# Performance work log

Hardware: AMD Instinct MI355X
Metric: run time of the kernel (lower is better)

The kernel has to match this reference:

```python
import jax, jax.numpy as jnp
import numpy as np

B, T, D, H, L = 2, 2048, 2048, 16, 64
HD = D // H  # 128
EPS = 1e-5


def setup_inputs() -> dict:
    key = jax.random.key(0)
    ks = jax.random.split(key, 16)
    s = 0.02
    inp = {
        'x': jax.random.normal(ks[0], (B, T, D), jnp.float32),
        'mask': jnp.tril(jnp.ones((T, T), dtype=bool)),
        'ln_w': jnp.ones((D,), jnp.float32),
        'ln_b': jnp.zeros((D,), jnp.float32),
        'wq': jax.random.normal(ks[1], (D, D), jnp.float32) * s,
        'bq': jnp.zeros((D,), jnp.float32),
        'wk': jax.random.normal(ks[2], (D, D), jnp.float32) * s,
        'bk': jnp.zeros((D,), jnp.float32),
        'wv': jax.random.normal(ks[3], (D, D), jnp.float32) * s,
        'bv': jnp.zeros((D,), jnp.float32),
        'wo': jax.random.normal(ks[4], (D, D), jnp.float32) * s,
        'bo': jnp.zeros((D,), jnp.float32),
        'wcq': jax.random.normal(ks[5], (HD, L), jnp.float32) * s,
        'bcq': jnp.zeros((L,), jnp.float32),
        'wck': jax.random.normal(ks[6], (HD, L), jnp.float32) * s,
        'bck': jnp.zeros((L,), jnp.float32),
        'wcv': jax.random.normal(ks[7], (HD, L), jnp.float32) * s,
        'bcv': jnp.zeros((L,), jnp.float32),
        'wd': jax.random.normal(ks[8], (L, HD), jnp.float32) * s,
        'bd': jnp.zeros((HD,), jnp.float32),
    }
    # standard RoPE frequency table: theta_i = 10000^{-2i/HD}
    inv_freq = 1.0 / (10000.0 ** (jnp.arange(0, HD, 2, dtype=jnp.float32) / HD))
    ang = jnp.arange(T, dtype=jnp.float32)[:, None] * inv_freq[None, :]  # [T, HD/2]
    inp['freqs_cos'] = jnp.cos(ang)
    inp['freqs_sin'] = jnp.sin(ang)
    return inp


def _rope(x, cos, sin):
    # x: [B,T,H,HD]; cos/sin: [T, HD/2]; interleaved (even=real, odd=imag)
    xr, xi = x[..., 0::2], x[..., 1::2]
    c = cos[None, :, None, :]
    sn = sin[None, :, None, :]
    out_r = xr * c - xi * sn
    out_i = xr * sn + xi * c
    return jnp.stack([out_r, out_i], axis=-1).reshape(x.shape)


def reference(x, mask, freqs_cos, freqs_sin, ln_w, ln_b, wq, bq, wk, bk, wv, bv,
              wo, bo, wcq, bcq, wck, bck, wcv, bcv, wd, bd):
    # LayerNorm
    mu = jnp.mean(x, axis=-1, keepdims=True)
    var = jnp.mean(jnp.square(x - mu), axis=-1, keepdims=True)
    xn = (x - mu) / jnp.sqrt(var + EPS) * ln_w + ln_b

    q = (xn @ wq + bq).reshape(B, T, H, HD)
    k = (xn @ wk + bk).reshape(B, T, H, HD)
    v = (xn @ wv + bv).reshape(B, T, H, HD)

    q, k = _rope(q, freqs_cos, freqs_sin), _rope(k, freqs_cos, freqs_sin)

    # compress each head to the latent dim
    q_lat = q @ wcq + bcq  # [B,T,H,L]
    k_lat = k @ wck + bck
    v_lat = v @ wcv + bcv

    scale = 1.0 / np.sqrt(L).astype(np.float32)
    scores = jnp.einsum('bqhl,bkhl->bhqk', q_lat, k_lat) * scale  # [B,H,T,T]
    additive = jnp.where(mask, 0.0, -1e9).astype(scores.dtype)  # bool mask -> additive
    scores = scores + additive[None, None, :, :]
    attn = jax.nn.softmax(scores, axis=-1)

    out = jnp.einsum('bhqk,bkhl->bqhl', attn, v_lat)  # [B,T,H,L]
    out = (out @ wd + bd).reshape(B, T, D)  # decompress to head_dim, merge heads
    return out @ wo + bo
```

## Files before the change

kernel.cpp:

```cpp
#include <hip/hip_runtime.h>
#include <hip/hip_bf16.h>
#include <stdint.h>

#define BB 2
#define TB 2048
#define DB 2048
#define HB 16
#define HDB 128
#define LB 64
#define MB 4096

typedef __hip_bfloat16 bf16;
typedef __attribute__((ext_vector_type(8))) short bf16x8;
typedef __attribute__((ext_vector_type(4))) float f32x4;

#define MFMA_16x16x32 __builtin_amdgcn_mfma_f32_16x16x32_bf16

typedef __attribute__((address_space(3))) void lds_t;
typedef const __attribute__((address_space(1))) void gvm_t;

static __device__ __forceinline__ float bf2f(bf16 h) { return __bfloat162float(h); }
static __device__ __forceinline__ bf16 f2bf(float f) { return __float2bfloat16(f); }
union BV8 { bf16x8 v; bf16 e[8]; };
static __device__ __forceinline__ float bfel(bf16x8 v, int e) { BV8 u; u.v = v; return bf2f(u.e[e]); }

#define SWZC(r) (((r) ^ ((r) >> 3)) & 7)

__global__ __launch_bounds__(256) void ln_kernel(const float* __restrict__ x,
                                                 const float* __restrict__ g,
                                                 const float* __restrict__ be,
                                                 bf16* __restrict__ xn) {
  int row = blockIdx.x, tid = threadIdx.x;
  const float4* xr = (const float4*)(x + (size_t)row * DB);
  float4 a = xr[2 * tid], b = xr[2 * tid + 1];
  float s = a.x + a.y + a.z + a.w + b.x + b.y + b.z + b.w;
  float s2 = a.x * a.x + a.y * a.y + a.z * a.z + a.w * a.w +
             b.x * b.x + b.y * b.y + b.z * b.z + b.w * b.w;
  for (int off = 32; off > 0; off >>= 1) {
    s += __shfl_down(s, off);
    s2 += __shfl_down(s2, off);
  }
  __shared__ float red[8];
  int w = tid >> 6, lane = tid & 63;
  if (lane == 0) { red[w] = s; red[4 + w] = s2; }
  __syncthreads();
  s = red[0] + red[1] + red[2] + red[3];
  s2 = red[4] + red[5] + red[6] + red[7];
  float mu = s * (1.f / DB);
  float var = s2 * (1.f / DB) - mu * mu;
  float rstd = rsqrtf(var + 1e-5f);
  const float4* gw = (const float4*)g;
  const float4* bb = (const float4*)be;
  float4 g0 = gw[2 * tid], g1 = gw[2 * tid + 1];
  float4 b0 = bb[2 * tid], b1 = bb[2 * tid + 1];
  BV8 u;
  u.e[0] = f2bf((a.x - mu) * rstd * g0.x + b0.x);
  u.e[1] = f2bf((a.y - mu) * rstd * g0.y + b0.y);
  u.e[2] = f2bf((a.z - mu) * rstd * g0.z + b0.z);
  u.e[3] = f2bf((a.w - mu) * rstd * g0.w + b0.w);
  u.e[4] = f2bf((b.x - mu) * rstd * g1.x + b1.x);
  u.e[5] = f2bf((b.y - mu) * rstd * g1.y + b1.y);
  u.e[6] = f2bf((b.z - mu) * rstd * g1.z + b1.z);
  u.e[7] = f2bf((b.w - mu) * rstd * g1.w + b1.w);
  *(bf16x8*)(xn + (size_t)row * DB + tid * 8) = u.v;
}

__global__ __launch_bounds__(256) void wconv_kernel(const float* __restrict__ W,
                                                    bf16* __restrict__ Wt) {
  __shared__ float t[32][33];
  int c0 = blockIdx.x * 32, r0 = blockIdx.y * 32;
  int tx = threadIdx.x & 31, ty = threadIdx.x >> 5;
  for (int p = 0; p < 4; ++p)
    t[ty + 8 * p][tx] = W[(size_t)(r0 + ty + 8 * p) * DB + c0 + tx];
  __syncthreads();
  for (int p = 0; p < 4; ++p)
    Wt[(size_t)(c0 + ty + 8 * p) * DB + r0 + tx] = f2bf(t[tx][ty + 8 * p]);
}

__global__ __launch_bounds__(256) void fold_v_kernel(const float* __restrict__ wv,
                                                     const float* __restrict__ wcv,
                                                     bf16* __restrict__ BtV) {
  __shared__ float wvs[128][36];
  int tid = threadIdx.x;
  int k0 = blockIdx.x * 128, h = blockIdx.y;
  int l = tid & 63, ks = tid >> 6;
  float acc[32];
#pragma unroll
  for (int i = 0; i < 32; ++i) acc[i] = 0.f;
  for (int dc = 0; dc < 128; dc += 32) {
    __syncthreads();
    for (int i = tid; i < 128 * 32; i += 256) {
      int kk = i >> 5, dd = i & 31;
      wvs[kk][dd] = wv[(size_t)(k0 + kk) * DB + h * 128 + dc + dd];
    }
    __syncthreads();
    float wr[32];
#pragma unroll
    for (int dd = 0; dd < 32; ++dd) wr[dd] = wcv[(dc + dd) * 64 + l];
#pragma unroll
    for (int i = 0; i < 32; ++i) {
      const float4* row = (const float4*)&wvs[ks * 32 + i][0];
#pragma unroll
      for (int d4 = 0; d4 < 8; ++d4) {
        float4 w4 = row[d4];
        acc[i] += w4.x * wr[d4 * 4] + w4.y * wr[d4 * 4 + 1] +
                  w4.z * wr[d4 * 4 + 2] + w4.w * wr[d4 * 4 + 3];
      }
    }
  }
  bf16* dst = BtV + (size_t)(h * 64 + l) * DB + k0 + ks * 32;
#pragma unroll
  for (int i8 = 0; i8 < 4; ++i8) {
    BV8 u;
#pragma unroll
    for (int j = 0; j < 8; ++j) u.e[j] = f2bf(acc[i8 * 8 + j]);
    *(bf16x8*)(dst + i8 * 8) = u.v;
  }
}

__global__ __launch_bounds__(256) void fold_o_kernel(const float* __restrict__ wo,
                                                     const float* __restrict__ wd,
                                                     bf16* __restrict__ BtO) {
  __shared__ float wos[32][132];
  int tid = threadIdx.x;
  int n0 = blockIdx.x * 128, h = blockIdx.y;
  int l = tid & 63, ns = tid >> 6;
  float acc[32];
#pragma unroll
  for (int i = 0; i < 32; ++i) acc[i] = 0.f;
  for (int dc = 0; dc < 128; dc += 32) {
    __syncthreads();
    for (int i = tid; i < 32 * 128; i += 256) {
      int dd = i >> 7, nn = i & 127;
      wos[dd][nn] = wo[(size_t)(h * 128 + dc + dd) * DB + n0 + nn];
    }
    __syncthreads();
    float wr[32];
#pragma unroll
    for (int d4 = 0; d4 < 8; ++d4) {
      float4 w4 = *(const float4*)&wd[l * 128 + dc + d4 * 4];
      wr[d4 * 4] = w4.x; wr[d4 * 4 + 1] = w4.y;
      wr[d4 * 4 + 2] = w4.z; wr[d4 * 4 + 3] = w4.w;
    }
#pragma unroll
    for (int dd = 0; dd < 32; ++dd) {
      float w = wr[dd];
      const float4* row = (const float4*)&wos[dd][ns * 32];
#pragma unroll
      for (int i4 = 0; i4 < 8; ++i4) {
        float4 a4 = row[i4];
        acc[i4 * 4 + 0] += a4.x * w; acc[i4 * 4 + 1] += a4.y * w;
        acc[i4 * 4 + 2] += a4.z * w; acc[i4 * 4 + 3] += a4.w * w;
      }
    }
  }
#pragma unroll
  for (int i = 0; i < 32; ++i)
    BtO[(size_t)(n0 + ns * 32 + i) * 1024 + h * 64 + l] = f2bf(acc[i]);
}

__global__ __launch_bounds__(256) void biasv_kernel(const float* __restrict__ bv,
                                                    const float* __restrict__ wcv,
                                                    const float* __restrict__ bcv,
                                                    float* __restrict__ bvlat) {
  int j = blockIdx.x * 256 + threadIdx.x;
  int h = j >> 6, l = j & 63;
  float s = bcv[l];
  for (int d = 0; d < 128; ++d) s += bv[h * 128 + d] * wcv[d * 64 + l];
  bvlat[j] = s;
}

__global__ __launch_bounds__(256) void biaso_kernel(const float* __restrict__ bd,
                                                    const float* __restrict__ wo,
                                                    const float* __restrict__ bo,
                                                    float* __restrict__ bo2) {
  __shared__ float red[4][64];
  int t = threadIdx.x;
  int nl = t & 63, ks = t >> 6;
  int n = blockIdx.x * 64 + nl;
  float s = 0.f;
  for (int k = ks * 512; k < ks * 512 + 512; ++k)
    s += bd[k & 127] * wo[(size_t)k * DB + n];
  red[ks][nl] = s;
  __syncthreads();
  if (ks == 0) bo2[n] = bo[n] + red[0][nl] + red[1][nl] + red[2][nl] + red[3][nl];
}

__global__ __launch_bounds__(256) void gemm_qkv_kernel(
    const bf16* __restrict__ A, const bf16* __restrict__ wqkT,
    const bf16* __restrict__ BtV,
    const float* __restrict__ bq, const float* __restrict__ bk,
    const float* __restrict__ bvl,
    const float* __restrict__ wcq, const float* __restrict__ wck,
    const float* __restrict__ bcq, const float* __restrict__ bck,
    bf16* __restrict__ qlat, bf16* __restrict__ klat, bf16* __restrict__ vlatT,
    const float* __restrict__ fcos, const float* __restrict__ fsin) {
  constexpr int K = DB;
  __shared__ __align__(16) char smem[49152];
  bf16* As = (bf16*)smem;
  bf16* Bs = (bf16*)(smem + 8192);
  bf16* Qt = (bf16*)smem;
  bf16* Wt = (bf16*)(smem + 32768);
  int tid = threadIdx.x;
  int m0 = blockIdx.y * 128, n0 = blockIdx.x * 128;
  int w = tid >> 6, l = tid & 63;
  int wr = w >> 1, wc = w & 1;
  int lrow = l & 15, lk = (l >> 4) * 8, ck = l >> 4;
  const bf16* Bsrc = (n0 < 4096) ? (wqkT + (size_t)n0 * K)
                                 : (BtV + (size_t)(n0 - 4096) * K);
  int sel = n0 >> 11;

  if (sel < 2) {
    const float* wcp = sel == 0 ? wcq : wck;
    for (int i = tid; i < 8192; i += 256) {
      int d = i >> 6, j = i & 63;
      Wt[j * 128 + (((d >> 3) ^ (j & 7)) * 8) + (d & 7)] = f2bf(wcp[d * 64 + j]);
    }
  }

  f32x4 zero4 = {0.f, 0.f, 0.f, 0.f};
  f32x4 acc[4][4];
  for (int m = 0; m < 4; ++m)
    for (int n = 0; n < 4; ++n) acc[m][n] = zero4;

  for (int kk = 0; kk < K / 32; ++kk) {
    int k0 = kk * 32;
    __syncthreads();
#pragma unroll
    for (int i = 0; i < 2; ++i) {
      int c = i * 256 + tid;
      int r = c >> 2, cc = c & 3;
      int cb = i * 256 + (tid & ~63);
      __builtin_amdgcn_global_load_lds(
          (gvm_t*)&A[(size_t)(m0 + r) * K + k0 + cc * 8], (lds_t*)&As[cb * 8], 16, 0, 0);
      __builtin_amdgcn_global_load_lds(
          (gvm_t*)&Bsrc[(size_t)r * K + k0 + cc * 8], (lds_t*)&Bs[cb * 8], 16, 0, 0);
    }
    __syncthreads();
    bf16x8 af[4], bfr[4];
    for (int m = 0; m < 4; ++m)
      af[m] = *(bf16x8*)&As[(wr * 64 + m * 16 + lrow) * 32 + lk];
    for (int n = 0; n < 4; ++n)
      bfr[n] = *(bf16x8*)&Bs[(wc * 64 + n * 16 + lrow) * 32 + lk];
    for (int m = 0; m < 4; ++m)
      for (int n = 0; n < 4; ++n)
        acc[m][n] = MFMA_16x16x32(af[m], bfr[n], acc[m][n], 0, 0, 0);
  }

  int rg = 4 * (l >> 4), cl = l & 15;
  if (sel == 2) {
    for (int mf = 0; mf < 4; ++mf) {
      int rowb = m0 + wr * 64 + mf * 16 + rg;
      for (int nf = 0; nf < 4; ++nf) {
        int col = n0 + wc * 64 + nf * 16 + cl;
        int colV = col - 4096;
        float bv_ = bvl[colV];
        size_t vbase = ((size_t)((rowb >> 11) * HB + (colV >> 6)) * 64 + (colV & 63)) * TB
                       + (rowb & (TB - 1));
        for (int r = 0; r < 4; ++r)
          vlatT[vbase + r] = f2bf(acc[mf][nf][r] + bv_);
      }
    }
    return;
  }

  const float* bias = sel == 0 ? bq : bk;
  __syncthreads();
  for (int mf = 0; mf < 4; ++mf) {
    int rowb = m0 + wr * 64 + mf * 16 + rg;
    int rl0 = wr * 64 + mf * 16 + rg;
    for (int nf = 0; nf < 4; ++nf) {
      int col = n0 + wc * 64 + nf * 16 + cl;
      int colL = col & 2047;
      int cloc = wc * 64 + nf * 16 + cl;
      float bv_ = bias[colL];
      for (int r = 0; r < 4; ++r) {
        int rr = rowb + r;
        float v = acc[mf][nf][r] + bv_;
        float pv = __shfl_xor(v, 1);
        int t = rr & (TB - 1);
        int pi = (col & 127) >> 1;
        float c = fcos[t * 64 + pi], sn = fsin[t * 64 + pi];
        v = (col & 1) ? (pv * sn + v * c) : (v * c - pv * sn);
        int rl = rl0 + r;
        Qt[rl * 128 + ((((cloc >> 3) ^ (rl & 7)) * 8) + (cloc & 7))] = f2bf(v);
      }
    }
  }
  __syncthreads();
  f32x4 pacc[2][4];
#pragma unroll
  for (int mi = 0; mi < 2; ++mi)
#pragma unroll
    for (int nf = 0; nf < 4; ++nf) pacc[mi][nf] = zero4;
#pragma unroll
  for (int kc = 0; kc < 4; ++kc) {
    bf16x8 aq[2], bw[4];
#pragma unroll
    for (int mi = 0; mi < 2; ++mi) {
      int row = w * 32 + mi * 16 + lrow;
      aq[mi] = *(bf16x8*)&Qt[row * 128 + (((kc * 4 + ck) ^ (row & 7)) * 8)];
    }
#pragma unroll
    for (int nf = 0; nf < 4; ++nf) {
      int jrow = nf * 16 + lrow;
      bw[nf] = *(bf16x8*)&Wt[jrow * 128 + (((kc * 4 + ck) ^ (jrow & 7)) * 8)];
    }
#pragma unroll
    for (int mi = 0; mi < 2; ++mi)
#pragma unroll
      for (int nf = 0; nf < 4; ++nf)
        pacc[mi][nf] = MFMA_16x16x32(aq[mi], bw[nf], pacc[mi][nf], 0, 0, 0);
  }
  int head = (n0 & 2047) >> 7;
  const float* bias2 = sel == 0 ? bcq : bck;
  bf16* outp = sel == 0 ? qlat : klat;
#pragma unroll
  for (int mi = 0; mi < 2; ++mi)
#pragma unroll
    for (int nf = 0; nf < 4; ++nf) {
      int colj = nf * 16 + cl;
      float b2 = bias2[colj];
#pragma unroll
      for (int r = 0; r < 4; ++r) {
        int roG = m0 + w * 32 + mi * 16 + rg + r;
        outp[((size_t)roG * HB + head) * 64 + colj] = f2bf(pacc[mi][nf][r] + b2);
      }
    }
}

__global__ __launch_bounds__(256) void gemm_out_kernel(
    const bf16* __restrict__ A, const bf16* __restrict__ Bt,
    const float* __restrict__ bias, float* __restrict__ Cout) {
  constexpr int K = 1024, N = DB;
  __shared__ __align__(16) bf16 As[128 * 32];
  __shared__ __align__(16) bf16 Bs[128 * 32];
  int tid = threadIdx.x;
  int m0 = blockIdx.y * 128, n0 = blockIdx.x * 128;
  int w = tid >> 6, l = tid & 63;
  int wr = w >> 1, wc = w & 1;
  int lrow = l & 15, lk = (l >> 4) * 8;

  f32x4 zero4 = {0.f, 0.f, 0.f, 0.f};
  f32x4 acc[4][4];
  for (int m = 0; m < 4; ++m)
    for (int n = 0; n < 4; ++n) acc[m][n] = zero4;

  for (int kk = 0; kk < K / 32; ++kk) {
    int k0 = kk * 32;
    __syncthreads();
#pragma unroll
    for (int i = 0; i < 2; ++i) {
      int c = i * 256 + tid;
      int r = c >> 2, cc = c & 3;
      int cb = i * 256 + (tid & ~63);
      __builtin_amdgcn_global_load_lds(
          (gvm_t*)&A[(size_t)(m0 + r) * K + k0 + cc * 8], (lds_t*)&As[cb * 8], 16, 0, 0);
      __builtin_amdgcn_global_load_lds(
          (gvm_t*)&Bt[(size_t)(n0 + r) * K + k0 + cc * 8], (lds_t*)&Bs[cb * 8], 16, 0, 0);
    }
    __syncthreads();
    bf16x8 af[4], bfr[4];
    for (int m = 0; m < 4; ++m)
      af[m] = *(bf16x8*)&As[(wr * 64 + m * 16 + lrow) * 32 + lk];
    for (int n = 0; n < 4; ++n)
      bfr[n] = *(bf16x8*)&Bs[(wc * 64 + n * 16 + lrow) * 32 + lk];
    for (int m = 0; m < 4; ++m)
      for (int n = 0; n < 4; ++n)
        acc[m][n] = MFMA_16x16x32(af[m], bfr[n], acc[m][n], 0, 0, 0);
  }

  int rg = 4 * (l >> 4), cl = l & 15;
  for (int m = 0; m < 4; ++m) {
    int rowb = m0 + wr * 64 + m * 16 + rg;
    for (int n = 0; n < 4; ++n) {
      int col = n0 + wc * 64 + n * 16 + cl;
      float bv = bias[col];
      for (int r = 0; r < 4; ++r)
        Cout[(size_t)(rowb + r) * N + col] = acc[m][n][r] + bv;
    }
  }
}

__global__ __launch_bounds__(256) void attn_kernel(const bf16* __restrict__ qlat,
                                                   const bf16* __restrict__ klat,
                                                   const bf16* __restrict__ vlatT,
                                                   bf16* __restrict__ aout) {
  int tid = threadIdx.x, w = tid >> 6, l = tid & 63;
  int job = ((int)blockIdx.x & 7) * 64 + ((int)blockIdx.x >> 3);
  int bh = job >> 4, pair = job & 15;
  int h = bh & 15, b = bh >> 4;
  int lrow = l & 15, ck = l >> 4, hi4 = l >> 4;
  __shared__ __align__(16) bf16 Ks[64 * 64];
  __shared__ __align__(16) bf16 VsT[64 * 64];
  __shared__ __align__(16) bf16 Ps[4][16 * 64];
  f32x4 zero4 = {0.f, 0.f, 0.f, 0.f};

  for (int half = 0; half < 2; ++half) {
    int tile = half ? pair : 31 - pair;
    int q0 = tile * 64;
    const bf16* qp = qlat + ((size_t)(b * TB + q0 + w * 16 + lrow) * HB + h) * LB;
    bf16x8 qf0 = *(const bf16x8*)(qp + ck * 8);
    bf16x8 qf1 = *(const bf16x8*)(qp + 32 + ck * 8);
    float mr[4], lsum[4];
    f32x4 o[4];
    for (int r = 0; r < 4; ++r) { mr[r] = -1e30f; lsum[r] = 0.f; }
    for (int n = 0; n < 4; ++n) o[n] = zero4;

    for (int kt = 0; kt <= tile; ++kt) {
      int kv0 = kt * 64;
      __syncthreads();
#pragma unroll
      for (int i = 0; i < 2; ++i) {
        int c = i * 256 + tid;
        int row = c >> 3, ch = c & 7;
        int dst = (c & ~63) * 8;
        __builtin_amdgcn_global_load_lds(
            (gvm_t*)(klat + ((size_t)(b * TB + kv0 + row) * HB + h) * LB + ((ch ^ SWZC(row)) * 8)),
            (lds_t*)&Ks[dst], 16, 0, 0);
        __builtin_amdgcn_global_load_lds(
            (gvm_t*)(vlatT + ((size_t)bh * 64 + row) * TB + kv0 + ((ch ^ SWZC(row)) * 8)),
            (lds_t*)&VsT[dst], 16, 0, 0);
      }
      __syncthreads();
      f32x4 s[4];
      __builtin_amdgcn_s_setprio(1);
#pragma unroll
      for (int kg = 0; kg < 4; ++kg) {
        int row = kg * 16 + lrow;
        int sw = SWZC(row);
        bf16x8 kf0 = *(bf16x8*)&Ks[row * 64 + ((ck ^ sw) * 8)];
        bf16x8 kf1 = *(bf16x8*)&Ks[row * 64 + (((ck + 4) ^ sw) * 8)];
        f32x4 a = zero4;
        a = MFMA_16x16x32(qf0, kf0, a, 0, 0, 0);
        a = MFMA_16x16x32(qf1, kf1, a, 0, 0, 0);
        s[kg] = a;
      }
      __builtin_amdgcn_s_setprio(0);
      float sc[4][4];
      bool diag = (kt == tile);
#pragma unroll
      for (int kg = 0; kg < 4; ++kg)
#pragma unroll
        for (int r = 0; r < 4; ++r) {
          float v = s[kg][r] * 0.125f;
          if (diag) {
            int kvg = kv0 + kg * 16 + lrow;
            int qr = q0 + w * 16 + 4 * hi4 + r;
            if (kvg > qr) v = -1e30f;
          }
          sc[kg][r] = v;
        }
      float rm[4], f[4], psum[4];
#pragma unroll
      for (int r = 0; r < 4; ++r)
        rm[r] = fmaxf(fmaxf(sc[0][r], sc[1][r]), fmaxf(sc[2][r], sc[3][r]));
      for (int off = 8; off > 0; off >>= 1)
#pragma unroll
        for (int r = 0; r < 4; ++r) rm[r] = fmaxf(rm[r], __shfl_xor(rm[r], off));
#pragma unroll
      for (int r = 0; r < 4; ++r) {
        float mn = fmaxf(mr[r], rm[r]);
        f[r] = __expf(mr[r] - mn);
        mr[r] = mn;
      }
#pragma unroll
      for (int kg = 0; kg < 4; ++kg)
#pragma unroll
        for (int r = 0; r < 4; ++r) sc[kg][r] = __expf(sc[kg][r] - mr[r]);
#pragma unroll
      for (int r = 0; r < 4; ++r)
        psum[r] = sc[0][r] + sc[1][r] + sc[2][r] + sc[3][r];
      for (int off = 8; off > 0; off >>= 1)
#pragma unroll
        for (int r = 0; r < 4; ++r) psum[r] += __shfl_xor(psum[r], off);
#pragma unroll
      for (int r = 0; r < 4; ++r) lsum[r] = lsum[r] * f[r] + psum[r];
#pragma unroll
      for (int n = 0; n < 4; ++n) {
        f32x4 t = o[n];
        t[0] *= f[0]; t[1] *= f[1]; t[2] *= f[2]; t[3] *= f[3];
        o[n] = t;
      }
#pragma unroll
      for (int r = 0; r < 4; ++r) {
        int rq = 4 * hi4 + r;
        int sw8 = SWZC(rq) << 3;
#pragma unroll
        for (int kg = 0; kg < 4; ++kg)
          Ps[w][rq * 64 + ((kg * 16 + lrow) ^ sw8)] = f2bf(sc[kg][r]);
      }
      int swp = SWZC(lrow);
      bf16x8 pa0 = *(bf16x8*)&Ps[w][lrow * 64 + ((ck ^ swp) * 8)];
      bf16x8 pa1 = *(bf16x8*)&Ps[w][lrow * 64 + (((ck + 4) ^ swp) * 8)];
      __builtin_amdgcn_s_setprio(1);
#pragma unroll
      for (int n = 0; n < 4; ++n) {
        int row = n * 16 + lrow;
        int sw = SWZC(row);
        bf16x8 vf0 = *(bf16x8*)&VsT[row * 64 + ((ck ^ sw) * 8)];
        bf16x8 vf1 = *(bf16x8*)&VsT[row * 64 + (((ck + 4) ^ sw) * 8)];
        o[n] = MFMA_16x16x32(pa0, vf0, o[n], 0, 0, 0);
        o[n] = MFMA_16x16x32(pa1, vf1, o[n], 0, 0, 0);
      }
      __builtin_amdgcn_s_setprio(0);
    }
    float inv[4];
#pragma unroll
    for (int r = 0; r < 4; ++r) inv[r] = 1.f / lsum[r];
#pragma unroll
    for (int n = 0; n < 4; ++n)
#pragma unroll
      for (int r = 0; r < 4; ++r) {
        size_t row = (size_t)b * TB + q0 + w * 16 + 4 * hi4 + r;
        aout[(row * HB + h) * LB + n * 16 + lrow] = f2bf(o[n][r] * inv[r]);
      }
  }
}

extern "C" void kernel_launch(void* const* d_in, const int* in_sizes, int n_in,
                              void* d_out, int out_size, void* d_ws, size_t ws_size,
                              hipStream_t stream) {
  const float* x    = (const float*)d_in[0];
  const float* ln_w = (const float*)d_in[2];
  const float* ln_b = (const float*)d_in[3];
  const float* wq   = (const float*)d_in[4];
  const float* bq   = (const float*)d_in[5];
  const float* wk   = (const float*)d_in[6];
  const float* bk   = (const float*)d_in[7];
  const float* wv   = (const float*)d_in[8];
  const float* bv   = (const float*)d_in[9];
  const float* wo   = (const float*)d_in[10];
  const float* bo   = (const float*)d_in[11];
  const float* wcq  = (const float*)d_in[12];
  const float* bcq  = (const float*)d_in[13];
  const float* wck  = (const float*)d_in[14];
  const float* bck  = (const float*)d_in[15];
  const float* wcv  = (const float*)d_in[16];
  const float* bcv  = (const float*)d_in[17];
  const float* wd   = (const float*)d_in[18];
  const float* bd   = (const float*)d_in[19];
  const float* fcos = (const float*)d_in[20];
  const float* fsin = (const float*)d_in[21];

  char* ws = (char*)d_ws;
  bf16*  xn    = (bf16*)(ws);
  bf16*  wqkT  = (bf16*)(ws + 16777216);
  bf16*  BtV   = (bf16*)(ws + 33554432);
  bf16*  BtO   = (bf16*)(ws + 37748736);
  bf16*  qlat  = (bf16*)(ws + 41943040);
  bf16*  klat  = (bf16*)(ws + 58720256);
  bf16*  vlatT = (bf16*)(ws + 75497472);
  float* bvlat = (float*)(ws + 83886080);
  float* bo2   = (float*)(ws + 83890176);
  bf16*  aoutp = wqkT;

  dim3 tg(64, 64);

  ln_kernel<<<MB, 256, 0, stream>>>(x, ln_w, ln_b, xn);

  wconv_kernel<<<tg, 256, 0, stream>>>(wq, wqkT);
  wconv_kernel<<<tg, 256, 0, stream>>>(wk, wqkT + (size_t)2048 * 2048);
  fold_v_kernel<<<dim3(16, 16), 256, 0, stream>>>(wv, wcv, BtV);
  fold_o_kernel<<<dim3(16, 16), 256, 0, stream>>>(wo, wd, BtO);
  biasv_kernel<<<4, 256, 0, stream>>>(bv, wcv, bcv, bvlat);
  biaso_kernel<<<32, 256, 0, stream>>>(bd, wo, bo, bo2);

  gemm_qkv_kernel<<<dim3(40, 32), 256, 0, stream>>>(
      xn, wqkT, BtV, bq, bk, bvlat, wcq, wck, bcq, bck,
      qlat, klat, vlatT, fcos, fsin);

  attn_kernel<<<512, 256, 0, stream>>>(qlat, klat, vlatT, aoutp);

  gemm_out_kernel<<<dim3(16, 32), 256, 0, stream>>>(aoutp, BtO, bo2, (float*)d_out);
}
```

Baseline: 347.9 us.

## Precompute bf16 latent weights and use 128-row query tiles in attention

Adds a small kernel that converts wcq/wck to bf16 in transposed layout once, so the QKV GEMM blocks read the compression weights straight from global memory. This replaces the per-block fp32 conversion into LDS and cuts shared memory from 48KB to 32KB, which may allow more resident blocks. The attention kernel moves to 512-thread blocks covering 128 query rows, so each K/V tile loaded into LDS is shared by eight waves. The cost is that waves whose rows lie entirely below a causal key tile sit idle for that tile.

```diff
diff --git a/kernel.cpp b/kernel.cpp
--- a/kernel.cpp
+++ b/kernel.cpp
@@ -186,21 +186,30 @@
   if (ks == 0) bo2[n] = bo[n] + red[0][nl] + red[1][nl] + red[2][nl] + red[3][nl];
 }
 
+__global__ __launch_bounds__(256) void latw_kernel(const float* __restrict__ wcq,
+                                                   const float* __restrict__ wck,
+                                                   bf16* __restrict__ wcb) {
+  int i = blockIdx.x * 256 + threadIdx.x;
+  int s = i >> 13, r = i & 8191;
+  int j = r >> 7, d = r & 127;
+  const float* src = s ? wck : wcq;
+  wcb[i] = f2bf(src[d * 64 + j]);
+}
+
 __global__ __launch_bounds__(256) void gemm_qkv_kernel(
     const bf16* __restrict__ A, const bf16* __restrict__ wqkT,
     const bf16* __restrict__ BtV,
     const float* __restrict__ bq, const float* __restrict__ bk,
     const float* __restrict__ bvl,
-    const float* __restrict__ wcq, const float* __restrict__ wck,
+    const bf16* __restrict__ wcb,
     const float* __restrict__ bcq, const float* __restrict__ bck,
     bf16* __restrict__ qlat, bf16* __restrict__ klat, bf16* __restrict__ vlatT,
     const float* __restrict__ fcos, const float* __restrict__ fsin) {
   constexpr int K = DB;
-  __shared__ __align__(16) char smem[49152];
+  __shared__ __align__(16) char smem[32768];
   bf16* As = (bf16*)smem;
   bf16* Bs = (bf16*)(smem + 8192);
   bf16* Qt = (bf16*)smem;
-  bf16* Wt = (bf16*)(smem + 32768);
   int tid = threadIdx.x;
   int m0 = blockIdx.y * 128, n0 = blockIdx.x * 128;
   int w = tid >> 6, l = tid & 63;
@@ -209,14 +218,6 @@
   const bf16* Bsrc = (n0 < 4096) ? (wqkT + (size_t)n0 * K)
                                  : (BtV + (size_t)(n0 - 4096) * K);
   int sel = n0 >> 11;
-
-  if (sel < 2) {
-    const float* wcp = sel == 0 ? wcq : wck;
-    for (int i = tid; i < 8192; i += 256) {
-      int d = i >> 6, j = i & 63;
-      Wt[j * 128 + (((d >> 3) ^ (j & 7)) * 8) + (d & 7)] = f2bf(wcp[d * 64 + j]);
-    }
-  }
 
   f32x4 zero4 = {0.f, 0.f, 0.f, 0.f};
   f32x4 acc[4][4];
@@ -265,6 +266,7 @@
   }
 
   const float* bias = sel == 0 ? bq : bk;
+  const bf16* wcb_s = wcb + (size_t)sel * 8192;
   __syncthreads();
   for (int mf = 0; mf < 4; ++mf) {
     int rowb = m0 + wr * 64 + mf * 16 + rg;
@@ -302,10 +304,8 @@
       aq[mi] = *(bf16x8*)&Qt[row * 128 + (((kc * 4 + ck) ^ (row & 7)) * 8)];
     }
 #pragma unroll
-    for (int nf = 0; nf < 4; ++nf) {
-      int jrow = nf * 16 + lrow;
-      bw[nf] = *(bf16x8*)&Wt[jrow * 128 + (((kc * 4 + ck) ^ (jrow & 7)) * 8)];
-    }
+    for (int nf = 0; nf < 4; ++nf)
+      bw[nf] = *(const bf16x8*)&wcb_s[(nf * 16 + lrow) * 128 + (kc * 4 + ck) * 8];
 #pragma unroll
     for (int mi = 0; mi < 2; ++mi)
 #pragma unroll
@@ -382,39 +382,40 @@
   }
 }
 
-__global__ __launch_bounds__(256) void attn_kernel(const bf16* __restrict__ qlat,
+__global__ __launch_bounds__(512) void attn_kernel(const bf16* __restrict__ qlat,
                                                    const bf16* __restrict__ klat,
                                                    const bf16* __restrict__ vlatT,
                                                    bf16* __restrict__ aout) {
   int tid = threadIdx.x, w = tid >> 6, l = tid & 63;
-  int job = ((int)blockIdx.x & 7) * 64 + ((int)blockIdx.x >> 3);
-  int bh = job >> 4, pair = job & 15;
+  int job = ((int)blockIdx.x & 7) * 32 + ((int)blockIdx.x >> 3);
+  int bh = job >> 3, pair = job & 7;
   int h = bh & 15, b = bh >> 4;
-  int lrow = l & 15, ck = l >> 4, hi4 = l >> 4;
+  int lrow = l & 15, ck = l >> 4;
+  int rg = 4 * (l >> 4);
   __shared__ __align__(16) bf16 Ks[64 * 64];
   __shared__ __align__(16) bf16 VsT[64 * 64];
-  __shared__ __align__(16) bf16 Ps[4][16 * 64];
+  __shared__ __align__(16) bf16 Ps[8][16 * 64];
   f32x4 zero4 = {0.f, 0.f, 0.f, 0.f};
 
   for (int half = 0; half < 2; ++half) {
-    int tile = half ? pair : 31 - pair;
-    int q0 = tile * 64;
-    const bf16* qp = qlat + ((size_t)(b * TB + q0 + w * 16 + lrow) * HB + h) * LB;
+    int tile = half ? pair : 15 - pair;
+    int q0 = tile * 128;
+    int myrow0 = q0 + w * 16;
+    const bf16* qp = qlat + ((size_t)(b * TB + myrow0 + lrow) * HB + h) * LB;
     bf16x8 qf0 = *(const bf16x8*)(qp + ck * 8);
     bf16x8 qf1 = *(const bf16x8*)(qp + 32 + ck * 8);
     float mr[4], lsum[4];
     f32x4 o[4];
     for (int r = 0; r < 4; ++r) { mr[r] = -1e30f; lsum[r] = 0.f; }
     for (int n = 0; n < 4; ++n) o[n] = zero4;
-
-    for (int kt = 0; kt <= tile; ++kt) {
+    int nkt = 2 * tile + 2;
+
+    for (int kt = 0; kt < nkt; ++kt) {
       int kv0 = kt * 64;
       __syncthreads();
-#pragma unroll
-      for (int i = 0; i < 2; ++i) {
-        int c = i * 256 + tid;
-        int row = c >> 3, ch = c & 7;
-        int dst = (c & ~63) * 8;
+      {
+        int row = tid >> 3, ch = tid & 7;
+        int dst = (tid & ~63) * 8;
         __builtin_amdgcn_global_load_lds(
             (gvm_t*)(klat + ((size_t)(b * TB + kv0 + row) * HB + h) * LB + ((ch ^ SWZC(row)) * 8)),
             (lds_t*)&Ks[dst], 16, 0, 0);
@@ -423,6 +424,7 @@
             (lds_t*)&VsT[dst], 16, 0, 0);
       }
       __syncthreads();
+      if (kv0 > myrow0 + 15) continue;
       f32x4 s[4];
       __builtin_amdgcn_s_setprio(1);
 #pragma unroll
@@ -438,7 +440,7 @@
       }
       __builtin_amdgcn_s_setprio(0);
       float sc[4][4];
-      bool diag = (kt == tile);
+      bool diag = (kv0 + 63 > myrow0);
 #pragma unroll
       for (int kg = 0; kg < 4; ++kg)
 #pragma unroll
@@ -446,7 +448,7 @@
           float v = s[kg][r] * 0.125f;
           if (diag) {
             int kvg = kv0 + kg * 16 + lrow;
-            int qr = q0 + w * 16 + 4 * hi4 + r;
+            int qr = myrow0 + rg + r;
             if (kvg > qr) v = -1e30f;
           }
           sc[kg][r] = v;
@@ -484,7 +486,7 @@
       }
 #pragma unroll
       for (int r = 0; r < 4; ++r) {
-        int rq = 4 * hi4 + r;
+        int rq = rg + r;
         int sw8 = SWZC(rq) << 3;
 #pragma unroll
         for (int kg = 0; kg < 4; ++kg)
@@ -512,7 +514,7 @@
     for (int n = 0; n < 4; ++n)
 #pragma unroll
       for (int r = 0; r < 4; ++r) {
-        size_t row = (size_t)b * TB + q0 + w * 16 + 4 * hi4 + r;
+        size_t row = (size_t)b * TB + myrow0 + rg + r;
         aout[(row * HB + h) * LB + n * 16 + lrow] = f2bf(o[n][r] * inv[r]);
       }
   }
@@ -553,6 +555,7 @@
   bf16*  vlatT = (bf16*)(ws + 75497472);
   float* bvlat = (float*)(ws + 83886080);
   float* bo2   = (float*)(ws + 83890176);
+  bf16*  wcb   = (bf16*)(ws + 83898368);
   bf16*  aoutp = wqkT;
 
   dim3 tg(64, 64);
@@ -565,12 +568,13 @@
   fold_o_kernel<<<dim3(16, 16), 256, 0, stream>>>(wo, wd, BtO);
   biasv_kernel<<<4, 256, 0, stream>>>(bv, wcv, bcv, bvlat);
   biaso_kernel<<<32, 256, 0, stream>>>(bd, wo, bo, bo2);
+  latw_kernel<<<64, 256, 0, stream>>>(wcq, wck, wcb);
 
   gemm_qkv_kernel<<<dim3(40, 32), 256, 0, stream>>>(
-      xn, wqkT, BtV, bq, bk, bvlat, wcq, wck, bcq, bck,
+      xn, wqkT, BtV, bq, bk, bvlat, wcb, bcq, bck,
       qlat, klat, vlatT, fcos, fsin);
 
-  attn_kernel<<<512, 256, 0, stream>>>(qlat, klat, vlatT, aoutp);
+  attn_kernel<<<256, 512, 0, stream>>>(qlat, klat, vlatT, aoutp);
 
   gemm_out_kernel<<<dim3(16, 32), 256, 0, stream>>>(aoutp, BtO, bo2, (float*)d_out);
 }
```

Measured after the change: 363.8 us. 1.05x slower.

## Shrink QKV GEMM LDS by pre-converting latent weights and splitting epilogue

Applied to the files above, without the earlier changes.

Moves the fp32-to-bf16 conversion of the q/k latent compression weights into a separate small kernel that writes them to global memory, so the QKV GEMM no longer stages them in LDS. The RoPE and latent-projection epilogue now processes the 128-row tile in two 64-row halves, so only a 16KB Q staging buffer is needed. Shared memory per block drops from 48KB to 16KB, which could allow more resident blocks per CU. The cost is an extra kernel launch, latent weights read from global/cache inside the epilogue, and extra barriers with half the warps idle during each RoPE half.

```diff
diff --git a/kernel.cpp b/kernel.cpp
--- a/kernel.cpp
+++ b/kernel.cpp
@@ -186,21 +186,30 @@
   if (ks == 0) bo2[n] = bo[n] + red[0][nl] + red[1][nl] + red[2][nl] + red[3][nl];
 }
 
+__global__ __launch_bounds__(256) void latw_kernel(const float* __restrict__ wcq,
+                                                   const float* __restrict__ wck,
+                                                   bf16* __restrict__ wcb) {
+  int i = blockIdx.x * 256 + threadIdx.x;
+  int s = i >> 13, r = i & 8191;
+  int j = r >> 7, d = r & 127;
+  const float* src = s ? wck : wcq;
+  wcb[i] = f2bf(src[d * 64 + j]);
+}
+
 __global__ __launch_bounds__(256) void gemm_qkv_kernel(
     const bf16* __restrict__ A, const bf16* __restrict__ wqkT,
     const bf16* __restrict__ BtV,
     const float* __restrict__ bq, const float* __restrict__ bk,
     const float* __restrict__ bvl,
-    const float* __restrict__ wcq, const float* __restrict__ wck,
+    const bf16* __restrict__ wcb,
     const float* __restrict__ bcq, const float* __restrict__ bck,
     bf16* __restrict__ qlat, bf16* __restrict__ klat, bf16* __restrict__ vlatT,
     const float* __restrict__ fcos, const float* __restrict__ fsin) {
   constexpr int K = DB;
-  __shared__ __align__(16) char smem[49152];
+  __shared__ __align__(16) char smem[16384];
   bf16* As = (bf16*)smem;
   bf16* Bs = (bf16*)(smem + 8192);
   bf16* Qt = (bf16*)smem;
-  bf16* Wt = (bf16*)(smem + 32768);
   int tid = threadIdx.x;
   int m0 = blockIdx.y * 128, n0 = blockIdx.x * 128;
   int w = tid >> 6, l = tid & 63;
@@ -209,14 +218,6 @@
   const bf16* Bsrc = (n0 < 4096) ? (wqkT + (size_t)n0 * K)
                                  : (BtV + (size_t)(n0 - 4096) * K);
   int sel = n0 >> 11;
-
-  if (sel < 2) {
-    const float* wcp = sel == 0 ? wcq : wck;
-    for (int i = tid; i < 8192; i += 256) {
-      int d = i >> 6, j = i & 63;
-      Wt[j * 128 + (((d >> 3) ^ (j & 7)) * 8) + (d & 7)] = f2bf(wcp[d * 64 + j]);
-    }
-  }
 
   f32x4 zero4 = {0.f, 0.f, 0.f, 0.f};
   f32x4 acc[4][4];
@@ -265,68 +266,60 @@
   }
 
   const float* bias = sel == 0 ? bq : bk;
-  __syncthreads();
-  for (int mf = 0; mf < 4; ++mf) {
-    int rowb = m0 + wr * 64 + mf * 16 + rg;
-    int rl0 = wr * 64 + mf * 16 + rg;
-    for (int nf = 0; nf < 4; ++nf) {
-      int col = n0 + wc * 64 + nf * 16 + cl;
-      int colL = col & 2047;
-      int cloc = wc * 64 + nf * 16 + cl;
-      float bv_ = bias[colL];
-      for (int r = 0; r < 4; ++r) {
-        int rr = rowb + r;
-        float v = acc[mf][nf][r] + bv_;
-        float pv = __shfl_xor(v, 1);
-        int t = rr & (TB - 1);
-        int pi = (col & 127) >> 1;
-        float c = fcos[t * 64 + pi], sn = fsin[t * 64 + pi];
-        v = (col & 1) ? (pv * sn + v * c) : (v * c - pv * sn);
-        int rl = rl0 + r;
-        Qt[rl * 128 + ((((cloc >> 3) ^ (rl & 7)) * 8) + (cloc & 7))] = f2bf(v);
-      }
-    }
-  }
-  __syncthreads();
-  f32x4 pacc[2][4];
-#pragma unroll
-  for (int mi = 0; mi < 2; ++mi)
-#pragma unroll
-    for (int nf = 0; nf < 4; ++nf) pacc[mi][nf] = zero4;
-#pragma unroll
-  for (int kc = 0; kc < 4; ++kc) {
-    bf16x8 aq[2], bw[4];
-#pragma unroll
-    for (int mi = 0; mi < 2; ++mi) {
-      int row = w * 32 + mi * 16 + lrow;
-      aq[mi] = *(bf16x8*)&Qt[row * 128 + (((kc * 4 + ck) ^ (row & 7)) * 8)];
-    }
-#pragma unroll
-    for (int nf = 0; nf < 4; ++nf) {
-      int jrow = nf * 16 + lrow;
-      bw[nf] = *(bf16x8*)&Wt[jrow * 128 + (((kc * 4 + ck) ^ (jrow & 7)) * 8)];
-    }
-#pragma unroll
-    for (int mi = 0; mi < 2; ++mi)
-#pragma unroll
-      for (int nf = 0; nf < 4; ++nf)
-        pacc[mi][nf] = MFMA_16x16x32(aq[mi], bw[nf], pacc[mi][nf], 0, 0, 0);
-  }
-  int head = (n0 & 2047) >> 7;
+  const bf16* wcb_s = wcb + (size_t)sel * 8192;
   const float* bias2 = sel == 0 ? bcq : bck;
   bf16* outp = sel == 0 ? qlat : klat;
-#pragma unroll
-  for (int mi = 0; mi < 2; ++mi)
+  int head = (n0 & 2047) >> 7;
+  __syncthreads();
+#pragma unroll
+  for (int h2 = 0; h2 < 2; ++h2) {
+    if (wr == h2) {
+      for (int mf = 0; mf < 4; ++mf) {
+        int rl2 = mf * 16 + rg;
+        for (int nf = 0; nf < 4; ++nf) {
+          int col = n0 + wc * 64 + nf * 16 + cl;
+          int cloc = wc * 64 + nf * 16 + cl;
+          float bv_ = bias[col & 2047];
+          for (int r = 0; r < 4; ++r) {
+            int rr = m0 + h2 * 64 + rl2 + r;
+            float v = acc[mf][nf][r] + bv_;
+            float pv = __shfl_xor(v, 1);
+            int t = rr & (TB - 1);
+            int pi = (col & 127) >> 1;
+            float c = fcos[t * 64 + pi], sn = fsin[t * 64 + pi];
+            v = (col & 1) ? (pv * sn + v * c) : (v * c - pv * sn);
+            int rl = rl2 + r;
+            Qt[rl * 128 + ((((cloc >> 3) ^ (rl & 7)) * 8) + (cloc & 7))] = f2bf(v);
+          }
+        }
+      }
+    }
+    __syncthreads();
+    f32x4 pacc[4];
+#pragma unroll
+    for (int nf = 0; nf < 4; ++nf) pacc[nf] = zero4;
+#pragma unroll
+    for (int kc = 0; kc < 4; ++kc) {
+      int row = w * 16 + lrow;
+      bf16x8 aq = *(bf16x8*)&Qt[row * 128 + (((kc * 4 + ck) ^ (row & 7)) * 8)];
+#pragma unroll
+      for (int nf = 0; nf < 4; ++nf) {
+        bf16x8 bw = *(const bf16x8*)&wcb_s[(nf * 16 + lrow) * 128 + (kc * 4 + ck) * 8];
+        pacc[nf] = MFMA_16x16x32(aq, bw, pacc[nf], 0, 0, 0);
+      }
+    }
 #pragma unroll
     for (int nf = 0; nf < 4; ++nf) {
       int colj = nf * 16 + cl;
       float b2 = bias2[colj];
 #pragma unroll
       for (int r = 0; r < 4; ++r) {
-        int roG = m0 + w * 32 + mi * 16 + rg + r;
-        outp[((size_t)roG * HB + head) * 64 + colj] = f2bf(pacc[mi][nf][r] + b2);
-      }
-    }
+        int roG = m0 + h2 * 64 + w * 16 + rg + r;
+        outp[((size_t)roG * HB + head) * 64 + colj] = f2bf(pacc[nf][r] + b2);
+      }
+    }
+    __syncthreads();
+  }
 }
 
 __global__ __launch_bounds__(256) void gemm_out_kernel(
@@ -553,6 +546,7 @@
   bf16*  vlatT = (bf16*)(ws + 75497472);
   float* bvlat = (float*)(ws + 83886080);
   float* bo2   = (float*)(ws + 83890176);
+  bf16*  wcb   = (bf16*)(ws + 83898368);
   bf16*  aoutp = wqkT;
 
   dim3 tg(64, 64);
@@ -565,9 +559,10 @@
   fold_o_kernel<<<dim3(16, 16), 256, 0, stream>>>(wo, wd, BtO);
   biasv_kernel<<<4, 256, 0, stream>>>(bv, wcv, bcv, bvlat);
   biaso_kernel<<<32, 256, 0, stream>>>(bd, wo, bo, bo2);
+  latw_kernel<<<64, 256, 0, stream>>>(wcq, wck, wcb);
 
   gemm_qkv_kernel<<<dim3(40, 32), 256, 0, stream>>>(
-      xn, wqkT, BtV, bq, bk, bvlat, wcq, wck, bcq, bck,
+      xn, wqkT, BtV, bq, bk, bvlat, wcb, bcq, bck,
       qlat, klat, vlatT, fcos, fsin);
 
   attn_kernel<<<512, 256, 0, stream>>>(qlat, klat, vlatT, aoutp);
```

New measurement: 371.4 us. 6.8% more time.
